# Optimization experiments

Hardware: AMD Instinct MI355X
Metric: run time of the kernel (lower is better)

## Reference

```python
import jax, jax.numpy as jnp
import numpy as np

B, N, L, D, H, NLAYERS, V = 8, 1024, 16, 256, 4, 2, 32000
DH = D // H  # per-head dim


def setup_inputs() -> dict:
    key = jax.random.key(0)
    ks = jax.random.split(key, 7)
    cfg_adj = jax.random.randint(ks[0], (B, N, N), 0, 2, dtype=jnp.int32)
    cfg_nodes = jax.random.randint(ks[1], (B, N, L), 0, V, dtype=jnp.int32)
    cfg_len = jax.random.randint(ks[2], (B,), 1, N + 1, dtype=jnp.int32)
    emb = jax.random.normal(ks[3], (V, D), jnp.float32) * 0.02
    # xavier-ish scale for per-head projections and attention vectors
    W = jax.random.normal(ks[4], (NLAYERS, H, D, DH), jnp.float32) * np.float32(np.sqrt(2.0 / (D + DH)))
    a_src = jax.random.normal(ks[5], (NLAYERS, H, DH), jnp.float32) * 0.1
    a_dst = jax.random.normal(ks[6], (NLAYERS, H, DH), jnp.float32) * 0.1
    ln_scale = jnp.ones((NLAYERS, D), jnp.float32)
    ln_bias = jnp.zeros((NLAYERS, D), jnp.float32)
    return {"cfg_adj": cfg_adj, "cfg_nodes": cfg_nodes, "cfg_len": cfg_len,
            "emb": emb, "W": W, "a_src": a_src, "a_dst": a_dst,
            "ln_scale": ln_scale, "ln_bias": ln_bias}


def _layer_norm(x, scale, bias, eps=1e-5):
    mu = jnp.mean(x, axis=-1, keepdims=True)
    var = jnp.var(x, axis=-1, keepdims=True)
    return (x - mu) * jax.lax.rsqrt(var + eps) * scale + bias


def reference(cfg_adj, cfg_nodes, cfg_len, emb, W, a_src, a_dst, ln_scale, ln_bias):
    # node features: mean over token embeddings (dropout is identity in eval)
    node_feat = emb[cfg_nodes].mean(axis=2)                       # (B,N,D)
    # add self-loops once (repeated add+clamp in the original is idempotent)
    adj = jnp.minimum(cfg_adj + jnp.eye(N, dtype=cfg_adj.dtype)[None], 1)
    neg_mask = (adj == 0)[:, None]                                # (B,1,N,N)
    h = node_feat
    for l in range(NLAYERS):
        Wh = jnp.einsum('bnd,hdk->bhnk', h, W[l])                 # (B,H,N,DH)
        src = jnp.einsum('bhnk,hk->bhn', Wh, a_src[l])            # (B,H,N)
        dst = jnp.einsum('bhnk,hk->bhn', Wh, a_dst[l])            # (B,H,N)
        e = jax.nn.leaky_relu(src[:, :, :, None] + dst[:, :, None, :], 0.2)
        e = jnp.where(neg_mask, jnp.float32(-1e9), e)             # masked fill
        alpha = jax.nn.softmax(e, axis=-1)                        # (B,H,N,N)
        h_prime = jnp.einsum('bhnm,bhmk->bhnk', alpha, Wh)        # (B,H,N,DH)
        h_cat = jnp.transpose(h_prime, (0, 2, 1, 3)).reshape(B, N, D)
        h = _layer_norm(h + h_cat, ln_scale[l], ln_bias[l])
    return h, cfg_len
```

## Files before the change

### kernel.cpp

```cpp
#include <hip/hip_runtime.h>
#include <math.h>

#define B 8
#define N 1024
#define L 16
#define D 256
#define H 4
#define DH 64
#define NLAYERS 2
#define V 32000

typedef __attribute__((ext_vector_type(8))) short short8;
typedef __attribute__((ext_vector_type(4))) float f32x4;

union U8 { uint4 u; short8 s; };

__device__ inline unsigned short f2bf(float x) {
    unsigned u = __float_as_uint(x);
    u = (u + 0x7fff + ((u >> 16) & 1)) >> 16;
    return (unsigned short)u;
}
__device__ inline float bf2f(unsigned short x) {
    return __uint_as_float(((unsigned)x) << 16);
}


#define CONV_THREADS 512000
#define CONV_F4      2048000

__global__ __launch_bounds__(1024) void k_pre(const float* __restrict__ W,
                                              const int* __restrict__ len,
                                              const float* __restrict__ emb,
                                              unsigned short* __restrict__ WT_sw,
                                              unsigned short* __restrict__ emb_bf,
                                              float* __restrict__ out_len) {
    int bt = blockIdx.x, tid = threadIdx.x;
    if (bt < NLAYERS * H) {
        int lh = bt;
        const float* Wl = W + (size_t)lh * D * DH;
        int dh = tid & 63;
        int d0 = (tid >> 6) * 16;
#pragma unroll
        for (int i = 0; i < 16; ++i) {
            int d = d0 + i;
            WT_sw[(((size_t)lh * 8 + (d >> 5)) * 64 + dh) * 32 + (d & 31)] = f2bf(Wl[(size_t)d * DH + dh]);
        }
    } else if (bt == NLAYERS * H) {
        if (tid < B) out_len[tid] = (float)len[tid];
    } else {
        int idx = (bt - NLAYERS * H - 1) * 1024 + tid;
        const float4* e4 = (const float4*)emb;
        ushort4* o4 = (ushort4*)emb_bf;
#pragma unroll
        for (int k = 0; k < 4; ++k) {
            int j = idx + k * CONV_THREADS;
            float4 v = e4[j];
            ushort4 o;
            o.x = f2bf(v.x); o.y = f2bf(v.y); o.z = f2bf(v.z); o.w = f2bf(v.w);
            o4[j] = o;
        }
    }
}

__device__ inline void wh_tile(const unsigned short* hA_t,
                               const unsigned short* __restrict__ WT_l,
                               const float* __restrict__ asrc_l,
                               const float* __restrict__ adst_l,
                               unsigned short* __restrict__ WhT_out,
                               float* __restrict__ srcv_out,
                               float* __restrict__ dstv_out,
                               int b, int n0t, int hh, int lane) {
    int rowLane = lane & 15, quad = lane >> 4;
    int bh = b * H + hh;
    const unsigned short* abase = hA_t + rowLane * 32 + quad * 8;
    const unsigned short* bbase = WT_l + (size_t)hh * 16384 + rowLane * 32 + quad * 8;
    f32x4 acc[4] = {};
#pragma unroll
    for (int kc = 0; kc < 8; ++kc) {
        short8 af = *(const short8*)(abase + kc * 512);
#pragma unroll
        for (int c = 0; c < 4; ++c) {
            short8 bf = *(const short8*)(bbase + (size_t)kc * 2048 + c * 512);
            acc[c] = __builtin_amdgcn_mfma_f32_16x16x32_bf16(af, bf, acc[c], 0, 0, 0);
        }
    }
    int m0 = n0t + quad * 4;
    float ps[4] = {0.f, 0.f, 0.f, 0.f}, pd[4] = {0.f, 0.f, 0.f, 0.f};
#pragma unroll
    for (int c = 0; c < 4; ++c) {
        int dh = c * 16 + rowLane;
        ushort4 o;
        o.x = f2bf(acc[c][0]); o.y = f2bf(acc[c][1]);
        o.z = f2bf(acc[c][2]); o.w = f2bf(acc[c][3]);
        *(ushort4*)&WhT_out[(((size_t)bh * 32 + (m0 >> 5)) * 64 + dh) * 32 + (m0 & 31)] = o;
        float as = asrc_l[hh * DH + dh];
        float ad = adst_l[hh * DH + dh];
#pragma unroll
        for (int r = 0; r < 4; ++r) { ps[r] += acc[c][r] * as; pd[r] += acc[c][r] * ad; }
    }
#pragma unroll
    for (int off = 1; off < 16; off <<= 1) {
#pragma unroll
        for (int r = 0; r < 4; ++r) {
            ps[r] += __shfl_xor(ps[r], off, 64);
            pd[r] += __shfl_xor(pd[r], off, 64);
        }
    }
    if (rowLane == 0) {
#pragma unroll
        for (int r = 0; r < 4; ++r) {
            srcv_out[bh * N + m0 + r] = ps[r];
            dstv_out[bh * N + m0 + r] = pd[r];
        }
    }
}

__global__ __launch_bounds__(1024) void k_gp(const unsigned short* __restrict__ emb_bf,
                                             const int* __restrict__ nodes,
                                             const int* __restrict__ adj,
                                             unsigned short* __restrict__ h_sw,
                                             unsigned long long* __restrict__ pack,
                                             const unsigned short* __restrict__ WT0,
                                             const float* __restrict__ asrc0,
                                             const float* __restrict__ adst0,
                                             unsigned short* __restrict__ WhT0,
                                             float* __restrict__ srcv0,
                                             float* __restrict__ dstv0) {
    int bt = blockIdx.x, tid = threadIdx.x;
    int wg = tid >> 6, lane = tid & 63;
    if (bt >= 512) {
        int idx = bt - 512;
        int b = idx >> 6, n0 = (idx & 63) * 16;
        int n = n0 + wg;
        const int* arow = adj + ((size_t)(b * N + n)) * N;
        unsigned long long* prow = pack + ((size_t)(b * N + n)) * 16;
        int g16 = lane & 15;
#pragma unroll
        for (int it = 0; it < 4; ++it) {
            int m0 = it * 256 + lane * 4;
            int4 a = *(const int4*)(arow + m0);
            unsigned nib = (unsigned)((a.x != 0) || (m0 == n))
                         | ((unsigned)((a.y != 0) || (m0 + 1 == n)) << 1)
                         | ((unsigned)((a.z != 0) || (m0 + 2 == n)) << 2)
                         | ((unsigned)((a.w != 0) || (m0 + 3 == n)) << 3);
            unsigned long long v = (unsigned long long)nib << (g16 * 4);
            v |= __shfl_xor(v, 1, 64);
            v |= __shfl_xor(v, 2, 64);
            v |= __shfl_xor(v, 4, 64);
            v |= __shfl_xor(v, 8, 64);
            if (g16 == 0) prow[it * 4 + (lane >> 4)] = v;
        }
        return;
    }
    __shared__ __align__(16) int nodesLds[256];
    __shared__ __align__(16) unsigned short hA[8 * 16 * 32];
    int b = bt >> 6, nt = bt & 63, n0 = nt * 16;
    if (tid < 256) nodesLds[tid] = nodes[((size_t)(b * N + n0)) * L + tid];
    __syncthreads();
    {
        int l32 = lane & 31, hi = lane >> 5;
        int d8 = l32 * 8;
        const int* np = nodesLds + wg * L;
        float s[8] = {0.f, 0.f, 0.f, 0.f, 0.f, 0.f, 0.f, 0.f};
#pragma unroll
        for (int l = 0; l < 8; ++l) {
            int tok = np[l * 2 + hi];
            U8 v; v.u = *(const uint4*)&emb_bf[(size_t)tok * D + d8];
#pragma unroll
            for (int j = 0; j < 8; ++j) s[j] += bf2f(((const unsigned short*)&v)[j]);
        }
#pragma unroll
        for (int j = 0; j < 8; ++j) s[j] += __shfl_xor(s[j], 32, 64);
        if (hi == 0) {
            U8 o;
#pragma unroll
            for (int j = 0; j < 8; ++j) ((unsigned short*)&o)[j] = f2bf(s[j] * (1.0f / L));
            int off = (d8 >> 5) * 512 + wg * 32 + (d8 & 31);
            *(uint4*)&hA[off] = o.u;
            *(uint4*)&h_sw[((size_t)(b * 64 + nt) * 8) * 512 + off] = o.u;
        }
    }
    __syncthreads();
    if (wg < 4) wh_tile(hA, WT0, asrc0, adst0, WhT0, srcv0, dstv0, b, n0, wg, lane);
}

#define AT_XT1  17408
#define AT_PACK 34560
#define AT_HA   36608
#define AT_SSUM 44800
#define AT_SIZE 45312

template <int FINAL>
__global__ __launch_bounds__(512, 4) void k_attn2(const unsigned long long* __restrict__ pack,
                                                  const float* __restrict__ srcv_in,
                                                  const float* __restrict__ dstv_in,
                                                  const unsigned short* __restrict__ WhT_in,
                                                  unsigned short* __restrict__ h_sw,
                                                  const float* __restrict__ scale_l,
                                                  const float* __restrict__ bias_l,
                                                  const unsigned short* __restrict__ WT_next,
                                                  const float* __restrict__ asrc_n,
                                                  const float* __restrict__ adst_n,
                                                  unsigned short* __restrict__ WhT_out,
                                                  float* __restrict__ srcv_out,
                                                  float* __restrict__ dstv_out,
                                                  float* __restrict__ out) {
    __shared__ __align__(16) char smem[AT_SIZE];
    float* dsts = (float*)smem;
    float* xt0 = (float*)smem;
    float* xt1 = (float*)(smem + AT_XT1);
    unsigned long long* packs = (unsigned long long*)(smem + AT_PACK);
    unsigned short* hA = (unsigned short*)(smem + AT_HA);
    float* ssum = (float*)(smem + AT_SSUM);

    int tid = threadIdx.x;
    int bt = blockIdx.x;
    int b = bt >> 6, nt = bt & 63, n0 = nt * 16;
    int wg = tid >> 6, lane = tid & 63;
    int half = wg >> 2, hh = wg & 3;
    int rowLane = lane & 15, quad = lane >> 4;
    int bh = b * H + hh;

    {
        const float* dv = dstv_in + (size_t)bh * N + half * 512;
        *(float4*)(dsts + hh * 1024 + half * 512 + lane * 4) = *(const float4*)(dv + lane * 4);
        *(float4*)(dsts + hh * 1024 + half * 512 + 256 + lane * 4) = *(const float4*)(dv + 256 + lane * 4);
        if (tid < 256) packs[tid] = pack[((size_t)(b * N + n0 + (tid >> 4))) * 16 + (tid & 15)];
    }
    __syncthreads();

    float src = srcv_in[bh * N + n0 + rowLane];
    float mx = src > 0.f ? src : 0.2f * src;
    const unsigned* prow = (const unsigned*)packs + rowLane * 32 + half * 16;
    const unsigned short* wbase = WhT_in + (size_t)bh * 65536 + rowLane * 32 + quad * 8;
    const float* dw = dsts + hh * 1024 + half * 512 + quad * 8;

    f32x4 acc[4] = {};
    float sum0 = 0.f, sum1 = 0.f;
    short8 fb[2][4];
#pragma unroll
    for (int c = 0; c < 4; ++c)
        fb[0][c] = *(const short8*)(wbase + (size_t)(half * 16) * 2048 + c * 512);
#pragma unroll 2
    for (int t2 = 0; t2 < 16; ++t2) {
        int cb = t2 & 1;
        int t2n = (t2 + 1) & 15;
#pragma unroll
        for (int c = 0; c < 4; ++c)
            fb[cb ^ 1][c] = *(const short8*)(wbase + (size_t)(half * 16 + t2n) * 2048 + c * 512);
        unsigned bits = (prow[t2] >> (quad * 8)) & 0xffu;
        float4 d0 = *(const float4*)(dw + t2 * 32);
        float4 d1 = *(const float4*)(dw + t2 * 32 + 4);
        float dd[8] = {d0.x, d0.y, d0.z, d0.w, d1.x, d1.y, d1.z, d1.w};
        unsigned pk[4];
#pragma unroll
        for (int j2 = 0; j2 < 4; ++j2) {
            float ea = src + dd[2 * j2];
            float eb = src + dd[2 * j2 + 1];
            ea = ea > 0.f ? ea : 0.2f * ea;
            eb = eb > 0.f ? eb : 0.2f * eb;
            float pa = ((bits >> (2 * j2)) & 1) ? __expf(ea - mx) : 0.f;
            float pb = ((bits >> (2 * j2 + 1)) & 1) ? __expf(eb - mx) : 0.f;
            sum0 += pa; sum1 += pb;
            pk[j2] = (__float_as_uint(pb) & 0xffff0000u) | (__float_as_uint(pa) >> 16);
        }
        U8 u; u.u = make_uint4(pk[0], pk[1], pk[2], pk[3]);
        short8 af = u.s;
        acc[0] = __builtin_amdgcn_mfma_f32_16x16x32_bf16(af, fb[cb][0], acc[0], 0, 0, 0);
        acc[1] = __builtin_amdgcn_mfma_f32_16x16x32_bf16(af, fb[cb][1], acc[1], 0, 0, 0);
        acc[2] = __builtin_amdgcn_mfma_f32_16x16x32_bf16(af, fb[cb][2], acc[2], 0, 0, 0);
        acc[3] = __builtin_amdgcn_mfma_f32_16x16x32_bf16(af, fb[cb][3], acc[3], 0, 0, 0);
    }
    float sum = sum0 + sum1;
    sum += __shfl_xor(sum, 16, 64);
    sum += __shfl_xor(sum, 32, 64);
    if (quad == 0) ssum[wg * 16 + rowLane] = sum;
    __syncthreads();

    float inv[4];
#pragma unroll
    for (int r = 0; r < 4; ++r) {
        int rr = quad * 4 + r;
        inv[r] = 1.0f / (ssum[hh * 16 + rr] + ssum[(4 + hh) * 16 + rr]);
    }
    float* xtw = half ? xt1 : xt0;
#pragma unroll
    for (int c = 0; c < 4; ++c)
#pragma unroll
        for (int r = 0; r < 4; ++r)
            xtw[(quad * 4 + r) * 268 + hh * 64 + c * 16 + rowLane] = acc[c][r] * inv[r];
    __syncthreads();

    int row = tid >> 5, c8 = tid & 31;
    int d0c = c8 * 8;
    size_t hsb = ((size_t)(b * 64 + nt) * 8 + (c8 >> 2)) * 512 + row * 32 + (c8 & 3) * 8;
    U8 r0;
    r0.u = *(const uint4*)(h_sw + hsb);
    float4 xa0 = *(const float4*)(xt0 + row * 268 + d0c);
    float4 xa1 = *(const float4*)(xt0 + row * 268 + d0c + 4);
    float4 xb0 = *(const float4*)(xt1 + row * 268 + d0c);
    float4 xb1 = *(const float4*)(xt1 + row * 268 + d0c + 4);
    float xp[8] = {xa0.x + xb0.x, xa0.y + xb0.y, xa0.z + xb0.z, xa0.w + xb0.w,
                   xa1.x + xb1.x, xa1.y + xb1.y, xa1.z + xb1.z, xa1.w + xb1.w};
    float xv[8];
    float s = 0.f, s2 = 0.f;
#pragma unroll
    for (int j = 0; j < 8; ++j) {
        float x = bf2f(((const unsigned short*)&r0)[j]) + xp[j];
        xv[j] = x; s += x; s2 += x * x;
    }
#pragma unroll
    for (int off = 1; off < 32; off <<= 1) {
        s += __shfl_xor(s, off, 32);
        s2 += __shfl_xor(s2, off, 32);
    }
    float mu = s * (1.0f / D);
    float var = s2 * (1.0f / D) - mu * mu;
    float rstd = rsqrtf(var + 1e-5f);
    if (FINAL) {
        float* orow = out + ((size_t)(b * N) + n0 + row) * D + d0c;
#pragma unroll
        for (int k = 0; k < 2; ++k) {
            float4 sc = *(const float4*)(scale_l + d0c + k * 4);
            float4 bi = *(const float4*)(bias_l + d0c + k * 4);
            float4 y;
            y.x = (xv[k * 4 + 0] - mu) * rstd * sc.x + bi.x;
            y.y = (xv[k * 4 + 1] - mu) * rstd * sc.y + bi.y;
            y.z = (xv[k * 4 + 2] - mu) * rstd * sc.z + bi.z;
            y.w = (xv[k * 4 + 3] - mu) * rstd * sc.w + bi.w;
            *(float4*)(orow + k * 4) = y;
        }
    } else {
        U8 o0;
#pragma unroll
        for (int j = 0; j < 8; ++j) {
            float scv = scale_l[d0c + j];
            float biv = bias_l[d0c + j];
            ((unsigned short*)&o0)[j] = f2bf((xv[j] - mu) * rstd * scv + biv);
        }
        *(uint4*)(h_sw + hsb) = o0.u;
        *(uint4*)&hA[(c8 >> 2) * 512 + row * 32 + (c8 & 3) * 8] = o0.u;
        __syncthreads();
        if (wg < 4)
            wh_tile(hA, WT_next, asrc_n, adst_n, WhT_out, srcv_out, dstv_out, b, n0, wg, lane);
    }
}

extern "C" void kernel_launch(void* const* d_in, const int* in_sizes, int n_in,
                              void* d_out, int out_size, void* d_ws, size_t ws_size,
                              hipStream_t stream) {
    const int* cfg_adj = (const int*)d_in[0];
    const int* cfg_nodes = (const int*)d_in[1];
    const int* cfg_len = (const int*)d_in[2];
    const float* emb = (const float*)d_in[3];
    const float* W = (const float*)d_in[4];
    const float* a_src = (const float*)d_in[5];
    const float* a_dst = (const float*)d_in[6];
    const float* ln_scale = (const float*)d_in[7];
    const float* ln_bias = (const float*)d_in[8];
    float* out = (float*)d_out;
    float* ws = (float*)d_ws;

    float* srcv0 = ws;
    float* dstv0 = srcv0 + (size_t)B * H * N;
    float* srcv1 = dstv0 + (size_t)B * H * N;
    float* dstv1 = srcv1 + (size_t)B * H * N;
    unsigned short* h_sw = (unsigned short*)(dstv1 + (size_t)B * H * N);
    unsigned short* WhT0 = h_sw + (size_t)B * N * D;
    unsigned short* WhT1 = WhT0 + (size_t)B * H * DH * N;
    unsigned short* WT_sw = WhT1 + (size_t)B * H * DH * N;
    unsigned long long* pack = (unsigned long long*)(WT_sw + (size_t)NLAYERS * H * D * DH);
    unsigned short* emb_bf = (unsigned short*)(pack + (size_t)B * N * 16);

    k_pre<<<NLAYERS * H + 1 + 500, 1024, 0, stream>>>(W, cfg_len, emb, WT_sw, emb_bf,
                                                      out + (size_t)B * N * D);
    k_gp<<<1024, 1024, 0, stream>>>(emb_bf, cfg_nodes, cfg_adj, h_sw, pack,
                                    WT_sw, a_src, a_dst, WhT0, srcv0, dstv0);
    k_attn2<0><<<512, 512, 0, stream>>>(pack, srcv0, dstv0, WhT0, h_sw,
                                        ln_scale, ln_bias,
                                        WT_sw + (size_t)H * 16384,
                                        a_src + (size_t)H * DH, a_dst + (size_t)H * DH,
                                        WhT1, srcv1, dstv1, nullptr);
    k_attn2<1><<<512, 512, 0, stream>>>(pack, srcv1, dstv1, WhT1, h_sw,
                                        ln_scale + D, ln_bias + D,
                                        nullptr, nullptr, nullptr,
                                        nullptr, nullptr, nullptr, out);
}
```

Baseline: 173.2 us.

## Give each wave a full key range over two row tiles per block

The attention kernel previously split the 1024 key columns between two wave groups for the same 16 query rows, then combined partial sums and outputs through shared memory. Now each block covers 32 query rows with 256 blocks, and each wave group walks all 32 key chunks for its own 16 rows. This removes the cross-half reduction and one barrier, and lets all 8 waves run the Wh projection tile afterward. In exchange there are half as many blocks, each loop is twice as long, and the launch-bounds occupancy hint drops from 4 to 2, which could hurt latency hiding.

```diff
diff --git a/kernel.cpp b/kernel.cpp
--- a/kernel.cpp
+++ b/kernel.cpp
@@ -184,14 +184,12 @@
     if (wg < 4) wh_tile(hA, WT0, asrc0, adst0, WhT0, srcv0, dstv0, b, n0, wg, lane);
 }
 
-#define AT_XT1  17408
-#define AT_PACK 34560
-#define AT_HA   36608
-#define AT_SSUM 44800
-#define AT_SIZE 45312
+#define A3_PACK 34304
+#define A3_HA   38400
+#define A3_SIZE 46592
 
 template <int FINAL>
-__global__ __launch_bounds__(512, 4) void k_attn2(const unsigned long long* __restrict__ pack,
+__global__ __launch_bounds__(512, 2) void k_attn3(const unsigned long long* __restrict__ pack,
                                                   const float* __restrict__ srcv_in,
                                                   const float* __restrict__ dstv_in,
                                                   const unsigned short* __restrict__ WhT_in,
@@ -205,49 +203,47 @@
                                                   float* __restrict__ srcv_out,
                                                   float* __restrict__ dstv_out,
                                                   float* __restrict__ out) {
-    __shared__ __align__(16) char smem[AT_SIZE];
+    __shared__ __align__(16) char smem[A3_SIZE];
     float* dsts = (float*)smem;
-    float* xt0 = (float*)smem;
-    float* xt1 = (float*)(smem + AT_XT1);
-    unsigned long long* packs = (unsigned long long*)(smem + AT_PACK);
-    unsigned short* hA = (unsigned short*)(smem + AT_HA);
-    float* ssum = (float*)(smem + AT_SSUM);
+    unsigned long long* packs = (unsigned long long*)(smem + A3_PACK);
+    unsigned short* hAall = (unsigned short*)(smem + A3_HA);
 
     int tid = threadIdx.x;
     int bt = blockIdx.x;
-    int b = bt >> 6, nt = bt & 63, n0 = nt * 16;
+    int b = bt & 7, pr = bt >> 3;
+    int n0base = pr * 32;
     int wg = tid >> 6, lane = tid & 63;
-    int half = wg >> 2, hh = wg & 3;
+    int tg = wg >> 2, hh = wg & 3;
     int rowLane = lane & 15, quad = lane >> 4;
     int bh = b * H + hh;
+    int n0t = n0base + tg * 16;
 
     {
-        const float* dv = dstv_in + (size_t)bh * N + half * 512;
-        *(float4*)(dsts + hh * 1024 + half * 512 + lane * 4) = *(const float4*)(dv + lane * 4);
-        *(float4*)(dsts + hh * 1024 + half * 512 + 256 + lane * 4) = *(const float4*)(dv + 256 + lane * 4);
-        if (tid < 256) packs[tid] = pack[((size_t)(b * N + n0 + (tid >> 4))) * 16 + (tid & 15)];
-    }
-    __syncthreads();
-
-    float src = srcv_in[bh * N + n0 + rowLane];
+        const float* dv = dstv_in + (size_t)bh * N + tg * 512;
+        *(float4*)(dsts + hh * 1024 + tg * 512 + lane * 4) = *(const float4*)(dv + lane * 4);
+        *(float4*)(dsts + hh * 1024 + tg * 512 + 256 + lane * 4) = *(const float4*)(dv + 256 + lane * 4);
+        packs[tid] = pack[((size_t)(b * N + n0base + (tid >> 4))) * 16 + (tid & 15)];
+    }
+    __syncthreads();
+
+    float src = srcv_in[bh * N + n0t + rowLane];
     float mx = src > 0.f ? src : 0.2f * src;
-    const unsigned* prow = (const unsigned*)packs + rowLane * 32 + half * 16;
+    const unsigned* prow = (const unsigned*)packs + (tg * 16 + rowLane) * 32;
     const unsigned short* wbase = WhT_in + (size_t)bh * 65536 + rowLane * 32 + quad * 8;
-    const float* dw = dsts + hh * 1024 + half * 512 + quad * 8;
+    const float* dw = dsts + hh * 1024 + quad * 8;
 
     f32x4 acc[4] = {};
     float sum0 = 0.f, sum1 = 0.f;
     short8 fb[2][4];
 #pragma unroll
-    for (int c = 0; c < 4; ++c)
-        fb[0][c] = *(const short8*)(wbase + (size_t)(half * 16) * 2048 + c * 512);
+    for (int c = 0; c < 4; ++c) fb[0][c] = *(const short8*)(wbase + c * 512);
 #pragma unroll 2
-    for (int t2 = 0; t2 < 16; ++t2) {
+    for (int t2 = 0; t2 < 32; ++t2) {
         int cb = t2 & 1;
-        int t2n = (t2 + 1) & 15;
+        int t2n = (t2 + 1) & 31;
 #pragma unroll
         for (int c = 0; c < 4; ++c)
-            fb[cb ^ 1][c] = *(const short8*)(wbase + (size_t)(half * 16 + t2n) * 2048 + c * 512);
+            fb[cb ^ 1][c] = *(const short8*)(wbase + (size_t)t2n * 2048 + c * 512);
         unsigned bits = (prow[t2] >> (quad * 8)) & 0xffu;
         float4 d0 = *(const float4*)(dw + t2 * 32);
         float4 d1 = *(const float4*)(dw + t2 * 32 + 4);
@@ -274,16 +270,12 @@
     float sum = sum0 + sum1;
     sum += __shfl_xor(sum, 16, 64);
     sum += __shfl_xor(sum, 32, 64);
-    if (quad == 0) ssum[wg * 16 + rowLane] = sum;
-    __syncthreads();
-
     float inv[4];
 #pragma unroll
-    for (int r = 0; r < 4; ++r) {
-        int rr = quad * 4 + r;
-        inv[r] = 1.0f / (ssum[hh * 16 + rr] + ssum[(4 + hh) * 16 + rr]);
-    }
-    float* xtw = half ? xt1 : xt0;
+    for (int r = 0; r < 4; ++r) inv[r] = 1.0f / __shfl(sum, quad * 4 + r, 64);
+
+    __syncthreads();
+    float* xtw = (float*)smem + tg * 4288;
 #pragma unroll
     for (int c = 0; c < 4; ++c)
 #pragma unroll
@@ -291,36 +283,38 @@
             xtw[(quad * 4 + r) * 268 + hh * 64 + c * 16 + rowLane] = acc[c][r] * inv[r];
     __syncthreads();
 
-    int row = tid >> 5, c8 = tid & 31;
-    int d0c = c8 * 8;
-    size_t hsb = ((size_t)(b * 64 + nt) * 8 + (c8 >> 2)) * 512 + row * 32 + (c8 & 3) * 8;
-    U8 r0;
+    int tg2 = tid >> 8, rowg = tid & 255;
+    int row = rowg >> 4, g = rowg & 15;
+    int nt = pr * 2 + tg2;
+    const float* xtt = (float*)smem + tg2 * 4288;
+    size_t hsb = ((size_t)(b * 64 + nt) * 8 + (g >> 1)) * 512 + row * 32 + (g & 1) * 16;
+    U8 r0, r1;
     r0.u = *(const uint4*)(h_sw + hsb);
-    float4 xa0 = *(const float4*)(xt0 + row * 268 + d0c);
-    float4 xa1 = *(const float4*)(xt0 + row * 268 + d0c + 4);
-    float4 xb0 = *(const float4*)(xt1 + row * 268 + d0c);
-    float4 xb1 = *(const float4*)(xt1 + row * 268 + d0c + 4);
-    float xp[8] = {xa0.x + xb0.x, xa0.y + xb0.y, xa0.z + xb0.z, xa0.w + xb0.w,
-                   xa1.x + xb1.x, xa1.y + xb1.y, xa1.z + xb1.z, xa1.w + xb1.w};
-    float xv[8];
+    r1.u = *(const uint4*)(h_sw + hsb + 8);
+    float4 xr[4];
+#pragma unroll
+    for (int k = 0; k < 4; ++k) xr[k] = *(const float4*)(xtt + row * 268 + g * 16 + k * 4);
+    float xv[16];
     float s = 0.f, s2 = 0.f;
 #pragma unroll
-    for (int j = 0; j < 8; ++j) {
-        float x = bf2f(((const unsigned short*)&r0)[j]) + xp[j];
+    for (int j = 0; j < 16; ++j) {
+        unsigned short hv = (j < 8) ? ((const unsigned short*)&r0)[j] : ((const unsigned short*)&r1)[j - 8];
+        float x = bf2f(hv) + ((const float*)xr)[j];
         xv[j] = x; s += x; s2 += x * x;
     }
 #pragma unroll
-    for (int off = 1; off < 32; off <<= 1) {
-        s += __shfl_xor(s, off, 32);
-        s2 += __shfl_xor(s2, off, 32);
+    for (int off = 1; off < 16; off <<= 1) {
+        s += __shfl_xor(s, off, 64);
+        s2 += __shfl_xor(s2, off, 64);
     }
     float mu = s * (1.0f / D);
     float var = s2 * (1.0f / D) - mu * mu;
     float rstd = rsqrtf(var + 1e-5f);
+    int d0c = g * 16;
     if (FINAL) {
-        float* orow = out + ((size_t)(b * N) + n0 + row) * D + d0c;
-#pragma unroll
-        for (int k = 0; k < 2; ++k) {
+        float* orow = out + ((size_t)(b * N) + nt * 16 + row) * D + d0c;
+#pragma unroll
+        for (int k = 0; k < 4; ++k) {
             float4 sc = *(const float4*)(scale_l + d0c + k * 4);
             float4 bi = *(const float4*)(bias_l + d0c + k * 4);
             float4 y;
@@ -331,18 +325,23 @@
             *(float4*)(orow + k * 4) = y;
         }
     } else {
-        U8 o0;
-#pragma unroll
-        for (int j = 0; j < 8; ++j) {
+        U8 o0, o1;
+#pragma unroll
+        for (int j = 0; j < 16; ++j) {
             float scv = scale_l[d0c + j];
             float biv = bias_l[d0c + j];
-            ((unsigned short*)&o0)[j] = f2bf((xv[j] - mu) * rstd * scv + biv);
+            unsigned short yb = f2bf((xv[j] - mu) * rstd * scv + biv);
+            if (j < 8) ((unsigned short*)&o0)[j] = yb;
+            else ((unsigned short*)&o1)[j - 8] = yb;
         }
         *(uint4*)(h_sw + hsb) = o0.u;
-        *(uint4*)&hA[(c8 >> 2) * 512 + row * 32 + (c8 & 3) * 8] = o0.u;
+        *(uint4*)(h_sw + hsb + 8) = o1.u;
+        unsigned short* ha = hAall + tg2 * 4096 + (g >> 1) * 512 + row * 32 + (g & 1) * 16;
+        *(uint4*)ha = o0.u;
+        *(uint4*)(ha + 8) = o1.u;
         __syncthreads();
-        if (wg < 4)
-            wh_tile(hA, WT_next, asrc_n, adst_n, WhT_out, srcv_out, dstv_out, b, n0, wg, lane);
+        wh_tile(hAall + tg * 4096, WT_next, asrc_n, adst_n, WhT_out, srcv_out, dstv_out,
+                b, n0t, hh, lane);
     }
 }
 
@@ -376,12 +375,12 @@
                                                       out + (size_t)B * N * D);
     k_gp<<<1024, 1024, 0, stream>>>(emb_bf, cfg_nodes, cfg_adj, h_sw, pack,
                                     WT_sw, a_src, a_dst, WhT0, srcv0, dstv0);
-    k_attn2<0><<<512, 512, 0, stream>>>(pack, srcv0, dstv0, WhT0, h_sw,
+    k_attn3<0><<<256, 512, 0, stream>>>(pack, srcv0, dstv0, WhT0, h_sw,
                                         ln_scale, ln_bias,
                                         WT_sw + (size_t)H * 16384,
                                         a_src + (size_t)H * DH, a_dst + (size_t)H * DH,
                                         WhT1, srcv1, dstv1, nullptr);
-    k_attn2<1><<<512, 512, 0, stream>>>(pack, srcv1, dstv1, WhT1, h_sw,
+    k_attn3<1><<<256, 512, 0, stream>>>(pack, srcv1, dstv1, WhT1, h_sw,
                                         ln_scale + D, ln_bias + D,
                                         nullptr, nullptr, nullptr,
                                         nullptr, nullptr, nullptr, out);
```

Measured after the change: 173.1 us. About the same (-0.1%).
